# Kernel tuning notes

Measured on AMD Instinct MI355X. Metric: run time of the kernel, lower is better.

The kernel has to match this reference:

```python
import jax, jax.numpy as jnp
import numpy as np

BLOCK = 128
FP8_MAX = 448.0  # max finite value of float8_e4m3fn
EPS = 1e-12


def _qdq_act(x, bs=BLOCK):
    """Blockwise (1 x bs) FP8 quantize-dequantize along the last dim."""
    M, K = x.shape
    xb = x.reshape(M, K // bs, bs)
    amax = jnp.max(jnp.abs(xb), axis=-1, keepdims=True)          # [M, K/bs, 1]
    scale = jnp.maximum(amax, EPS) / FP8_MAX
    q = (xb / scale).astype(jnp.float8_e4m3fn)                   # fp8 rounding/saturation
    return (q.astype(jnp.float32) * scale).reshape(M, K)


def _qdq_weight(w, bs=BLOCK):
    """Blockwise (bs x bs) FP8 quantize-dequantize of weight [N, K]."""
    N, K = w.shape
    wb = w.reshape(N // bs, bs, K // bs, bs)
    amax = jnp.max(jnp.abs(wb), axis=(1, 3), keepdims=True)      # [N/bs,1,K/bs,1]
    scale = jnp.maximum(amax, EPS) / FP8_MAX
    q = (wb / scale).astype(jnp.float8_e4m3fn)
    return (q.astype(jnp.float32) * scale).reshape(N, K)


def setup_inputs() -> dict:
    key = jax.random.key(0)
    k1, k2 = jax.random.split(key)
    M, K, N = 8192, 4096, 11008
    x = jax.random.normal(k1, (M, K), dtype=jnp.float32)
    # kaiming_uniform_ default: bound = sqrt(6 / fan_in) with a=sqrt(5) gain folded -> use gain=sqrt(2/(1+5))
    bound = float(np.sqrt(6.0 / K) * np.sqrt(2.0 / 6.0))
    weight = jax.random.uniform(k2, (N, K), dtype=jnp.float32, minval=-bound, maxval=bound)
    bias = jnp.zeros((N,), dtype=jnp.float32)
    return {"input": x, "weight": weight, "bias": bias}


def reference(input, weight, bias):
    # FP8 blockwise quantized linear: dequant(Q(x)) @ dequant(Q(W)).T + b
    x_dq = _qdq_act(input)            # [M, K]
    w_dq = _qdq_weight(weight)        # [N, K]
    out = jnp.einsum('mk,nk->mn', x_dq, w_dq)  # [M, N]
    return out + bias[None, :]
```

## Files before the change

### kernel.cpp

```cpp
#include <hip/hip_runtime.h>
#include <stdint.h>

#define Mdim 8192
#define Kdim 4096
#define Ndim 11008
#define KBLK 32
#define NBLK 86
#define FP8MAX 448.0f
#define QEPS 1e-12f

typedef float v4f __attribute__((ext_vector_type(4)));

__device__ __forceinline__ void async16(void* lds, const void* g) {
  __builtin_amdgcn_global_load_lds(
      (const __attribute__((address_space(1))) unsigned int*)g,
      (__attribute__((address_space(3))) unsigned int*)lds, 16, 0, 0);
}

__global__ __launch_bounds__(256) void quant_x_kernel(const float* __restrict__ x,
                                                      uint8_t* __restrict__ qx,
                                                      float* __restrict__ sx) {
  const int tid = blockIdx.x * 256 + threadIdx.x;
  const int64_t base = (int64_t)tid * 4;
  const float4 v = *(const float4*)(x + base);
  float a = fmaxf(fmaxf(fabsf(v.x), fabsf(v.y)), fmaxf(fabsf(v.z), fabsf(v.w)));
#pragma unroll
  for (int off = 16; off >= 1; off >>= 1) a = fmaxf(a, __shfl_xor(a, off, 32));
  const float scale = fmaxf(a, QEPS) / FP8MAX;
  int p = __builtin_amdgcn_cvt_pk_fp8_f32(v.x / scale, v.y / scale, 0, false);
  p = __builtin_amdgcn_cvt_pk_fp8_f32(v.z / scale, v.w / scale, p, true);
  *(int*)(qx + base) = p;
  if ((threadIdx.x & 31) == 0) {
    const int blk = tid >> 5;
    const int m = blk >> 5;
    const int kb = blk & 31;
    sx[kb * Mdim + m] = scale;
  }
}

__global__ __launch_bounds__(256) void quant_w_kernel(const float* __restrict__ w,
                                                      uint8_t* __restrict__ qw,
                                                      float* __restrict__ sw) {
  const int kb = blockIdx.x, nb = blockIdx.y;
  const int t = threadIdx.x;
  const int r = t >> 1;
  const int c0 = (t & 1) * 64;
  const int64_t gbase = (int64_t)(nb * 128 + r) * Kdim + kb * 128 + c0;
  float4 v[16];
  float a = 0.0f;
#pragma unroll
  for (int i = 0; i < 16; ++i) {
    v[i] = *(const float4*)(w + gbase + i * 4);
    a = fmaxf(a, fmaxf(fmaxf(fabsf(v[i].x), fabsf(v[i].y)),
                       fmaxf(fabsf(v[i].z), fabsf(v[i].w))));
  }
#pragma unroll
  for (int off = 32; off >= 1; off >>= 1) a = fmaxf(a, __shfl_xor(a, off, 64));
  __shared__ float red[4];
  if ((t & 63) == 0) red[t >> 6] = a;
  __syncthreads();
  a = fmaxf(fmaxf(red[0], red[1]), fmaxf(red[2], red[3]));
  const float scale = fmaxf(a, QEPS) / FP8MAX;
#pragma unroll
  for (int i = 0; i < 16; ++i) {
    int p = __builtin_amdgcn_cvt_pk_fp8_f32(v[i].x / scale, v[i].y / scale, 0, false);
    p = __builtin_amdgcn_cvt_pk_fp8_f32(v[i].z / scale, v[i].w / scale, p, true);
    *(int*)(qw + gbase + i * 4) = p;
  }
  if (t == 0) sw[nb * KBLK + kb] = scale;
}

__global__ __launch_bounds__(256, 3) void gemm_kernel(
    const uint8_t* __restrict__ qx, const uint8_t* __restrict__ qw,
    const float* __restrict__ sx, const float* __restrict__ sw,
    const float* __restrict__ bias, float* __restrict__ out) {
  __shared__ __align__(16) uint8_t As[128 * 128];
  __shared__ __align__(16) uint8_t Bs[128 * 128];
  __shared__ __align__(16) float Ssx[KBLK][128];
  __shared__ float Ssw[KBLK];

  const int tid = threadIdx.x;
  const int wid = tid >> 6;
  const int lane = tid & 63;
  const int bn = blockIdx.x, bm = blockIdx.y;
  const int wm = wid >> 1, wn = wid & 1;
  const int m0 = bm * 128, n0 = bn * 128;
  const int lr = lane & 15;
  const int lq = lane >> 4;
  const int cbase = (lq * 8) ^ ((lr & 7) << 4);

  const v4f zero4 = {0.f, 0.f, 0.f, 0.f};
  v4f acc[4][4];
#pragma unroll
  for (int i = 0; i < 4; ++i)
#pragma unroll
    for (int j = 0; j < 4; ++j) acc[i][j] = zero4;

#pragma unroll
  for (int rr = 0; rr < 4; ++rr) {
    const int f = tid + rr * 256;
    const int kb = f >> 5;
    const int mrel = (f & 31) * 4;
    *(v4f*)&Ssx[kb][mrel] = *(const v4f*)(sx + (int64_t)kb * Mdim + m0 + mrel);
  }
  if (tid < KBLK) Ssw[tid] = sw[bn * KBLK + tid];

  const int srow = tid >> 3;
  const int scol = ((tid & 7) << 4) ^ ((srow & 7) << 4);
  const uint8_t* gA = qx + (int64_t)(m0 + srow) * Kdim + scol;
  const uint8_t* gB = qw + (int64_t)(n0 + srow) * Kdim + scol;
  uint8_t* ldsA = As + wid * 1024;
  uint8_t* ldsB = Bs + wid * 1024;

  for (int kb = 0; kb < KBLK; ++kb) {
    const int koff = kb * 128;
#pragma unroll
    for (int j = 0; j < 4; ++j) {
      async16(ldsA + j * 4096, gA + (int64_t)(j * 32) * Kdim + koff);
      async16(ldsB + j * 4096, gB + (int64_t)(j * 32) * Kdim + koff);
    }
    __syncthreads();

    long long bfr[4][4];
#pragma unroll
    for (int ks = 0; ks < 4; ++ks)
#pragma unroll
      for (int j = 0; j < 4; ++j)
        bfr[ks][j] = *(const long long*)(Bs + (wn * 64 + j * 16 + lr) * 128 +
                                         ((ks * 32) ^ cbase));

    const float sww = Ssw[kb];
#pragma unroll
    for (int i = 0; i < 4; ++i) {
      const int arow = (wm * 64 + i * 16 + lr) * 128;
      const long long a0 = *(const long long*)(As + arow + ((0) ^ cbase));
      const long long a1 = *(const long long*)(As + arow + ((32) ^ cbase));
      const long long a2 = *(const long long*)(As + arow + ((64) ^ cbase));
      const long long a3 = *(const long long*)(As + arow + ((96) ^ cbase));
      v4f s4 = *(const v4f*)&Ssx[kb][wm * 64 + i * 16 + lq * 4];
      s4 *= sww;
#pragma unroll
      for (int j = 0; j < 4; ++j) {
        v4f t = __builtin_amdgcn_mfma_f32_16x16x32_fp8_fp8(a0, bfr[0][j], zero4, 0, 0, 0);
        t = __builtin_amdgcn_mfma_f32_16x16x32_fp8_fp8(a1, bfr[1][j], t, 0, 0, 0);
        t = __builtin_amdgcn_mfma_f32_16x16x32_fp8_fp8(a2, bfr[2][j], t, 0, 0, 0);
        t = __builtin_amdgcn_mfma_f32_16x16x32_fp8_fp8(a3, bfr[3][j], t, 0, 0, 0);
        acc[i][j] += s4 * t;
      }
    }
    __syncthreads();
  }

#pragma unroll
  for (int i = 0; i < 4; ++i) {
    const int grow = m0 + wm * 64 + i * 16 + lq * 4;
#pragma unroll
    for (int j = 0; j < 4; ++j) {
      const int gcol = n0 + wn * 64 + j * 16 + lr;
      const float bv = bias[gcol];
      float* p = out + (int64_t)grow * Ndim + gcol;
      p[0] = acc[i][j][0] + bv;
      p[Ndim] = acc[i][j][1] + bv;
      p[2 * Ndim] = acc[i][j][2] + bv;
      p[3 * Ndim] = acc[i][j][3] + bv;
    }
  }
}

extern "C" void kernel_launch(void* const* d_in, const int* in_sizes, int n_in,
                              void* d_out, int out_size, void* d_ws, size_t ws_size,
                              hipStream_t stream) {
  const float* x = (const float*)d_in[0];
  const float* w = (const float*)d_in[1];
  const float* bias = (const float*)d_in[2];
  float* out = (float*)d_out;

  uint8_t* ws = (uint8_t*)d_ws;
  uint8_t* qx = ws;
  uint8_t* qw = qx + (size_t)Mdim * Kdim;
  float* sx = (float*)(qw + (size_t)Ndim * Kdim);
  float* sw = sx + (size_t)KBLK * Mdim;

  quant_x_kernel<<<(Mdim / 256) * (Kdim / 4), 256, 0, stream>>>(x, qx, sx);
  quant_w_kernel<<<dim3(KBLK, NBLK), 256, 0, stream>>>(w, qw, sw);
  gemm_kernel<<<dim3(NBLK, Mdim / 128), 256, 0, stream>>>(qx, qw, sx, sw, bias, out);
}
```

Measured before the change: 1.105 ms.

## Use 16x16x128 scaled FP8 MFMA and widen quantization kernel accesses

Replaces each chain of four 16x16x32 FP8 MFMAs with a single gfx950 mfma_scale 16x16x128 f8f6f4 instruction, using unit scales (0x7F exponent), and loads A/B fragments as two 16-byte LDS reads instead of four 8-byte reads. The quantization kernels are restructured so each thread handles 16 contiguous activation elements, and weight threads read row-coalesced float4 across 128 columns. The aim is fewer MFMA issues and LDS instructions in the GEMM and better memory coalescing in the quant passes. The fragment layout for the K=128 instruction must match the swizzled LDS layout for results to stay correct.

```diff
diff --git a/kernel.cpp b/kernel.cpp
--- a/kernel.cpp
+++ b/kernel.cpp
@@ -10,6 +10,8 @@
 #define QEPS 1e-12f
 
 typedef float v4f __attribute__((ext_vector_type(4)));
+typedef int v4i __attribute__((ext_vector_type(4)));
+typedef int v8i __attribute__((ext_vector_type(8)));
 
 __device__ __forceinline__ void async16(void* lds, const void* g) {
   __builtin_amdgcn_global_load_lds(
@@ -21,17 +23,28 @@
                                                       uint8_t* __restrict__ qx,
                                                       float* __restrict__ sx) {
   const int tid = blockIdx.x * 256 + threadIdx.x;
-  const int64_t base = (int64_t)tid * 4;
-  const float4 v = *(const float4*)(x + base);
-  float a = fmaxf(fmaxf(fabsf(v.x), fabsf(v.y)), fmaxf(fabsf(v.z), fabsf(v.w)));
-#pragma unroll
-  for (int off = 16; off >= 1; off >>= 1) a = fmaxf(a, __shfl_xor(a, off, 32));
+  const int64_t base = (int64_t)tid * 16;
+  float4 v[4];
+  float a = 0.0f;
+#pragma unroll
+  for (int i = 0; i < 4; ++i) {
+    v[i] = *(const float4*)(x + base + i * 4);
+    a = fmaxf(a, fmaxf(fmaxf(fabsf(v[i].x), fabsf(v[i].y)),
+                       fmaxf(fabsf(v[i].z), fabsf(v[i].w))));
+  }
+#pragma unroll
+  for (int off = 4; off >= 1; off >>= 1) a = fmaxf(a, __shfl_xor(a, off, 8));
   const float scale = fmaxf(a, QEPS) / FP8MAX;
-  int p = __builtin_amdgcn_cvt_pk_fp8_f32(v.x / scale, v.y / scale, 0, false);
-  p = __builtin_amdgcn_cvt_pk_fp8_f32(v.z / scale, v.w / scale, p, true);
-  *(int*)(qx + base) = p;
-  if ((threadIdx.x & 31) == 0) {
-    const int blk = tid >> 5;
+  v4i q;
+#pragma unroll
+  for (int i = 0; i < 4; ++i) {
+    int p = __builtin_amdgcn_cvt_pk_fp8_f32(v[i].x / scale, v[i].y / scale, 0, false);
+    p = __builtin_amdgcn_cvt_pk_fp8_f32(v[i].z / scale, v[i].w / scale, p, true);
+    q[i] = p;
+  }
+  *(v4i*)(qx + base) = q;
+  if ((threadIdx.x & 7) == 0) {
+    const int blk = tid >> 3;
     const int m = blk >> 5;
     const int kb = blk & 31;
     sx[kb * Mdim + m] = scale;
@@ -43,16 +56,16 @@
                                                       float* __restrict__ sw) {
   const int kb = blockIdx.x, nb = blockIdx.y;
   const int t = threadIdx.x;
-  const int r = t >> 1;
-  const int c0 = (t & 1) * 64;
-  const int64_t gbase = (int64_t)(nb * 128 + r) * Kdim + kb * 128 + c0;
+  const int rs = t >> 5;
+  const int cc = (t & 31) * 4;
+  const float* wb = w + (int64_t)(nb * 128) * Kdim + kb * 128;
   float4 v[16];
   float a = 0.0f;
 #pragma unroll
-  for (int i = 0; i < 16; ++i) {
-    v[i] = *(const float4*)(w + gbase + i * 4);
-    a = fmaxf(a, fmaxf(fmaxf(fabsf(v[i].x), fabsf(v[i].y)),
-                       fmaxf(fabsf(v[i].z), fabsf(v[i].w))));
+  for (int s = 0; s < 16; ++s) {
+    v[s] = *(const float4*)(wb + (int64_t)(s * 8 + rs) * Kdim + cc);
+    a = fmaxf(a, fmaxf(fmaxf(fabsf(v[s].x), fabsf(v[s].y)),
+                       fmaxf(fabsf(v[s].z), fabsf(v[s].w))));
   }
 #pragma unroll
   for (int off = 32; off >= 1; off >>= 1) a = fmaxf(a, __shfl_xor(a, off, 64));
@@ -61,11 +74,12 @@
   __syncthreads();
   a = fmaxf(fmaxf(red[0], red[1]), fmaxf(red[2], red[3]));
   const float scale = fmaxf(a, QEPS) / FP8MAX;
-#pragma unroll
-  for (int i = 0; i < 16; ++i) {
-    int p = __builtin_amdgcn_cvt_pk_fp8_f32(v[i].x / scale, v[i].y / scale, 0, false);
-    p = __builtin_amdgcn_cvt_pk_fp8_f32(v[i].z / scale, v[i].w / scale, p, true);
-    *(int*)(qw + gbase + i * 4) = p;
+  uint8_t* qb = qw + (int64_t)(nb * 128) * Kdim + kb * 128;
+#pragma unroll
+  for (int s = 0; s < 16; ++s) {
+    int p = __builtin_amdgcn_cvt_pk_fp8_f32(v[s].x / scale, v[s].y / scale, 0, false);
+    p = __builtin_amdgcn_cvt_pk_fp8_f32(v[s].z / scale, v[s].w / scale, p, true);
+    *(int*)(qb + (int64_t)(s * 8 + rs) * Kdim + cc) = p;
   }
   if (t == 0) sw[nb * KBLK + kb] = scale;
 }
@@ -87,7 +101,9 @@
   const int m0 = bm * 128, n0 = bn * 128;
   const int lr = lane & 15;
   const int lq = lane >> 4;
-  const int cbase = (lq * 8) ^ ((lr & 7) << 4);
+  const int cswz = (lr & 7) << 4;
+  const int c0 = (lq * 32) ^ cswz;
+  const int c1 = (lq * 32 + 16) ^ cswz;
 
   const v4f zero4 = {0.f, 0.f, 0.f, 0.f};
   v4f acc[4][4];
@@ -121,30 +137,28 @@
     }
     __syncthreads();
 
-    long long bfr[4][4];
-#pragma unroll
-    for (int ks = 0; ks < 4; ++ks)
-#pragma unroll
-      for (int j = 0; j < 4; ++j)
-        bfr[ks][j] = *(const long long*)(Bs + (wn * 64 + j * 16 + lr) * 128 +
-                                         ((ks * 32) ^ cbase));
+    v8i bfr[4];
+#pragma unroll
+    for (int j = 0; j < 4; ++j) {
+      const uint8_t* bp = Bs + (wn * 64 + j * 16 + lr) * 128;
+      v4i lo = *(const v4i*)(bp + c0);
+      v4i hi = *(const v4i*)(bp + c1);
+      bfr[j] = __builtin_shufflevector(lo, hi, 0, 1, 2, 3, 4, 5, 6, 7);
+    }
 
     const float sww = Ssw[kb];
 #pragma unroll
     for (int i = 0; i < 4; ++i) {
-      const int arow = (wm * 64 + i * 16 + lr) * 128;
-      const long long a0 = *(const long long*)(As + arow + ((0) ^ cbase));
-      const long long a1 = *(const long long*)(As + arow + ((32) ^ cbase));
-      const long long a2 = *(const long long*)(As + arow + ((64) ^ cbase));
-      const long long a3 = *(const long long*)(As + arow + ((96) ^ cbase));
+      const uint8_t* ap = As + (wm * 64 + i * 16 + lr) * 128;
+      v4i lo = *(const v4i*)(ap + c0);
+      v4i hi = *(const v4i*)(ap + c1);
+      v8i af = __builtin_shufflevector(lo, hi, 0, 1, 2, 3, 4, 5, 6, 7);
       v4f s4 = *(const v4f*)&Ssx[kb][wm * 64 + i * 16 + lq * 4];
       s4 *= sww;
 #pragma unroll
       for (int j = 0; j < 4; ++j) {
-        v4f t = __builtin_amdgcn_mfma_f32_16x16x32_fp8_fp8(a0, bfr[0][j], zero4, 0, 0, 0);
-        t = __builtin_amdgcn_mfma_f32_16x16x32_fp8_fp8(a1, bfr[1][j], t, 0, 0, 0);
-        t = __builtin_amdgcn_mfma_f32_16x16x32_fp8_fp8(a2, bfr[2][j], t, 0, 0, 0);
-        t = __builtin_amdgcn_mfma_f32_16x16x32_fp8_fp8(a3, bfr[3][j], t, 0, 0, 0);
+        v4f t = __builtin_amdgcn_mfma_scale_f32_16x16x128_f8f6f4(
+            af, bfr[j], zero4, 0, 0, 0, 0x7F7F7F7F, 0, 0x7F7F7F7F);
         acc[i][j] += s4 * t;
       }
     }
@@ -152,12 +166,12 @@
   }
 
 #pragma unroll
-  for (int i = 0; i < 4; ++i) {
-    const int grow = m0 + wm * 64 + i * 16 + lq * 4;
-#pragma unroll
-    for (int j = 0; j < 4; ++j) {
-      const int gcol = n0 + wn * 64 + j * 16 + lr;
-      const float bv = bias[gcol];
+  for (int j = 0; j < 4; ++j) {
+    const int gcol = n0 + wn * 64 + j * 16 + lr;
+    const float bv = bias[gcol];
+#pragma unroll
+    for (int i = 0; i < 4; ++i) {
+      const int grow = m0 + wm * 64 + i * 16 + lq * 4;
       float* p = out + (int64_t)grow * Ndim + gcol;
       p[0] = acc[i][j][0] + bv;
       p[Ndim] = acc[i][j][1] + bv;
@@ -181,7 +195,7 @@
   float* sx = (float*)(qw + (size_t)Ndim * Kdim);
   float* sw = sx + (size_t)KBLK * Mdim;
 
-  quant_x_kernel<<<(Mdim / 256) * (Kdim / 4), 256, 0, stream>>>(x, qx, sx);
+  quant_x_kernel<<<(Mdim * Kdim / 16) / 256, 256, 0, stream>>>(x, qx, sx);
   quant_w_kernel<<<dim3(KBLK, NBLK), 256, 0, stream>>>(w, qw, sw);
   gemm_kernel<<<dim3(NBLK, Mdim / 128), 256, 0, stream>>>(qx, qw, sx, sw, bias, out);
 }
```

Measured after the change: 1.014 ms. 8.2% less time.
